# Optimization experiments

Hardware: AMD Instinct MI355X
Metric: run time of the kernel (lower is better)

## Reference

```python
import jax, jax.numpy as jnp
import numpy as np

# block index -> upsample target resolution / whether self-attention is applied
RES = [32, 64, 256, 128, 64, 32, 16, 16, 32, 64, 128, 256]
ATTN = [False, False, False, False, False, True, True, True, True, False, False, False]
EPS = 1e-5


def conv5(x, w, b):
    # valid 5x5 conv, NCHW
    y = jax.lax.conv_general_dilated(x, w, (1, 1), 'VALID',
                                     dimension_numbers=('NCHW', 'OIHW', 'NCHW'))
    return y + b[None, :, None, None]


def up_nearest(x, size):
    # torch nn.Upsample(size) nearest: src_idx = floor(dst_idx * in / out)
    H, W = x.shape[2], x.shape[3]
    ri = (jnp.arange(size) * H) // size
    ci = (jnp.arange(size) * W) // size
    return x[:, :, ri][:, :, :, ci]


def norm_hw(x):
    # InstanceNorm2d(affine=False) == LayerNorm((H,W)) with identity affine:
    # normalize over spatial dims per (N, C), biased variance.
    m = x.mean((2, 3), keepdims=True)
    v = x.var((2, 3), keepdims=True)
    return (x - m) * jax.lax.rsqrt(v + EPS)


def norm_batch(x):
    # BatchNorm2d in training mode: batch statistics over (N, H, W) per channel.
    m = x.mean((0, 2, 3), keepdims=True)
    v = x.var((0, 2, 3), keepdims=True)
    return (x - m) * jax.lax.rsqrt(v + EPS)


def attention(x, qw, qb, kw, kb, vw, vb):
    B, C, H, W = x.shape
    q = (jnp.einsum('oc,bchw->bohw', qw, x) + qb[None, :, None, None]).reshape(B, C, H * W)
    k = (jnp.einsum('oc,bchw->bohw', kw, x) + kb[None, :, None, None]).reshape(B, C, H * W)
    v = (jnp.einsum('oc,bchw->bohw', vw, x) + vb[None, :, None, None]).reshape(B, C, H * W)
    # scores[b, m, n] = sum_c k[b, c, m] * q[b, c, n]; softmax over n
    a = jax.nn.softmax(jnp.einsum('bcm,bcn->bmn', k, q), axis=-1)  # [B, HW, HW]
    out = jnp.einsum('bcm,bmn->bcn', v, a).reshape(B, C, H, W)
    return out + x


def setup_inputs() -> dict:
    key = jax.random.key(0)
    k = jax.random.split(key, 22)
    s = 0.1
    f = jnp.float32
    return {
        'x': jax.random.normal(k[0], (32, 3, 256, 256), f),
        'noise_z': jax.random.normal(k[1], (1, 512), f),
        'lin_w': jax.random.normal(k[2], (768, 512), f) * 0.02,
        'lin_b': jax.random.normal(k[3], (768,), f) * 0.02,
        'conv_w': jax.random.normal(k[4], (12, 3, 3, 5, 5), f) * s,
        'conv_b': jax.random.normal(k[5], (12, 3), f) * s,
        'conv2_w': jax.random.normal(k[6], (12, 3, 3, 5, 5), f) * s,
        'conv2_b': jax.random.normal(k[7], (12, 3), f) * s,
        'q_w': jax.random.normal(k[8], (12, 3, 3), f) * s,
        'q_b': jax.random.normal(k[9], (12, 3), f) * s,
        'k_w': jax.random.normal(k[10], (12, 3, 3), f) * s,
        'k_b': jax.random.normal(k[11], (12, 3), f) * s,
        'v_w': jax.random.normal(k[12], (12, 3, 3), f) * s,
        'v_b': jax.random.normal(k[13], (12, 3), f) * s,
        'in_p': jax.random.uniform(k[14], (12, 3), f),
        'ln_p': jax.random.uniform(k[15], (12, 3), f),
        'bn_p': jax.random.uniform(k[16], (12, 3), f),
        'bn_w': jax.random.uniform(k[17], (12, 3), f),
        'bn_b': jax.random.uniform(k[18], (12, 3), f) * 0.1,
        'p1': jax.random.uniform(k[19], (12,), f),
        'p2': jax.random.uniform(k[20], (12,), f),
    }


def reference(x, noise_z, lin_w, lin_b, conv_w, conv_b, conv2_w, conv2_b,
              q_w, q_b, k_w, k_b, v_w, v_b, in_p, ln_p, bn_p, bn_w, bn_b, p1, p2):

    def block(i, h):
        r = RES[i]
        real = h
        y = up_nearest(conv5(real, conv_w[i], conv_b[i]), r)
        # InstanceNorm / LayerNorm (no affine) coincide here; BatchNorm has affine.
        inorm = norm_hw(y)
        bnorm = norm_batch(y) * bn_w[i][None, :, None, None] + bn_b[i][None, :, None, None]
        y2 = y + (jnp.sum(in_p[i]) + jnp.sum(ln_p[i])) * inorm + jnp.sum(bn_p[i]) * bnorm
        y2 = y2 * p1[i] + p2[i] * up_nearest(conv5(real, conv2_w[i], conv2_b[i]), r)
        if ATTN[i]:
            y2 = attention(y2, q_w[i], q_b[i], k_w[i], k_b[i], v_w[i], v_b[i])
        return y2

    # noise path: Linear(512 -> 768) -> (1, 3, 16, 16) -> ReesBlock(32) -> ReesBlock(64)
    n = (noise_z @ lin_w.T + lin_b).reshape(1, 3, 16, 16)
    n = block(0, n)
    n = block(1, n)  # (1, 3, 64, 64)

    a = x
    for i in range(2, 12):
        a = block(i, a)
        if i == 4:  # encoder index 2, resolution 64 -> add noise (broadcast over batch)
            a = a + n
    return jnp.tanh(a)
```

## Files before the change

kernel.cpp:

```cpp
#include <hip/hip_runtime.h>
#include <math.h>

#define EPS 1e-5f
#define LOG2E 1.44269504088896340736f

#define AS_GLOBAL __attribute__((address_space(1)))
#define AS_LDS    __attribute__((address_space(3)))

__device__ __forceinline__ float2 ab_from(float s1, float s2, float bs, float bs2,
    float hw, float Nf, float si_, float sb, float bnw_c, float bnb_c, float p1v) {
  float inv = 1.0f / hw;
  float mi = s1 * inv, vi = s2 * inv - mi * mi;
  float ri = rsqrtf(vi + EPS);
  float invb = 1.0f / (Nf * hw);
  float mb = bs * invb, vb = bs2 * invb - mb * mb;
  float rb = rsqrtf(vb + EPS);
  float A = 1.0f + si_ * ri + sb * rb * bnw_c;
  float B = -(si_ * ri * mi + sb * rb * bnw_c * mb) + sb * bnb_c;
  return make_float2(A * p1v, B * p1v);
}

__device__ __forceinline__ void compute_AB_P(
    const float* __restrict__ P, int n, int NT, int T, float hw, float Nf,
    const float* __restrict__ inp, const float* __restrict__ lnp,
    const float* __restrict__ bnp, const float* __restrict__ bnw,
    const float* __restrict__ bnb, const float* __restrict__ p1p,
    const float* __restrict__ p2p, float* pA, float* pB, float* pP2,
    float* sred ) {
  int t = threadIdx.x;
  if (t == 0) *pP2 = p2p[0];
  if (t < 192) {
    int c2 = t >> 5, l = t & 31;
    const float* pp = P + c2 * NT;
    float aAll = 0.f, aOwn = 0.f;
    int base = n * T;
    #pragma unroll 4
    for (int i = l; i < NT; i += 32) {
      float v = pp[i];
      aAll += v;
      if ((unsigned)(i - base) < (unsigned)T) aOwn += v;
    }
    #pragma unroll
    for (int off = 16; off; off >>= 1) {
      aAll += __shfl_down(aAll, off, 32);
      aOwn += __shfl_down(aOwn, off, 32);
    }
    if (l == 0) { sred[c2] = aOwn; sred[6 + c2] = aAll; }
  }
  __syncthreads();
  if (t < 3) {
    int c = t;
    float si_ = inp[0] + inp[1] + inp[2] + lnp[0] + lnp[1] + lnp[2];
    float sb = bnp[0] + bnp[1] + bnp[2];
    float2 ab = ab_from(sred[2 * c], sred[2 * c + 1], sred[6 + 2 * c],
                        sred[6 + 2 * c + 1], hw, Nf, si_, sb, bnw[c], bnb[c],
                        p1p[0]);
    pA[c] = ab.x;
    pB[c] = ab.y;
  }
  __syncthreads();
}

#define STATS_REDUCE_STORE(scv, sqv, sumsp, bidv)                             \
  {                                                                           \
    _Pragma("unroll")                                                         \
    for (int off = 32; off; off >>= 1) {                                      \
      _Pragma("unroll")                                                       \
      for (int c = 0; c < 3; ++c) {                                           \
        scv[c] += __shfl_down(scv[c], off);                                   \
        sqv[c] += __shfl_down(sqv[c], off);                                   \
      }                                                                       \
    }                                                                         \
    __shared__ float redS[4][3], redQ[4][3];                                  \
    int wid = threadIdx.x >> 6, lane = threadIdx.x & 63;                      \
    if (lane == 0) {                                                          \
      _Pragma("unroll")                                                       \
      for (int c = 0; c < 3; ++c) { redS[wid][c] = scv[c]; redQ[wid][c] = sqv[c]; } \
    }                                                                         \
    __syncthreads();                                                          \
    if (threadIdx.x < 3) {                                                    \
      int c = threadIdx.x;                                                    \
      int NTg = (int)gridDim.x;                                               \
      sumsp[(2 * c) * NTg + (bidv)] =                                         \
          redS[0][c] + redS[1][c] + redS[2][c] + redS[3][c];                  \
      sumsp[(2 * c + 1) * NTg + (bidv)] =                                     \
          redQ[0][c] + redQ[1][c] + redQ[2][c] + redQ[3][c];                  \
    }                                                                         \
  }

__device__ __forceinline__ int xcd_swz() {
  return ((int)(blockIdx.x & 7)) * ((int)gridDim.x >> 3) + ((int)blockIdx.x >> 3);
}

template <int MODE, bool IDENT>
__device__ __forceinline__ void stage_tile(
    float* __restrict__ lin, const float* __restrict__ inb, size_t ps,
    const float2* __restrict__ pyu, size_t pbase,
    int Hin, int sy0, int sx0, int Sp, int logrp,
    const float* pA, const float* pB, float pP2v,
    const float* __restrict__ pnoise) {
  const int IW = 68, IH = 20;
  int colt = threadIdx.x & 63;
  int r4 = threadIdx.x >> 6;
  int gx = sx0 + colt; gx = gx < Hin ? gx : Hin - 1;
  int gxs = (MODE == 1) ? (IDENT ? gx : ((gx * Sp) >> logrp)) : 0;
  #pragma unroll
  for (int cc = 0; cc < 3; ++cc) {
    #pragma unroll
    for (int rb = 0; rb < 5; ++rb) {
      int rr = r4 + (rb << 2);
      int gy = sy0 + rr; gy = gy < Hin ? gy : Hin - 1;
      float val;
      if (MODE == 1) {
        int rbase = IDENT ? gy * Sp : ((gy * Sp) >> logrp) * Sp;
        float2 v = pyu[pbase + (size_t)cc * Sp * Sp + rbase + gxs];
        val = pA[cc] * v.x + pB[cc] + pP2v * v.y;
        if (pnoise) val += pnoise[((size_t)cc * Hin + gy) * Hin + gx];
      } else if (MODE == 2) {
        size_t idx = ((size_t)cc * Hin + gy) * Hin + gx;
        val = inb[idx] + inb[idx + ps] + inb[idx + 2 * ps] + inb[idx + 3 * ps];
      } else {
        val = inb[((size_t)cc * Hin + gy) * Hin + gx];
      }
      lin[(cc * IH + rr) * IW + colt] = val;
    }
  }
  if (threadIdx.x < 240) {
    int col2 = 64 + (threadIdx.x & 3);
    int rowlin = threadIdx.x >> 2;
    int cc = rowlin / 20, rr = rowlin - cc * 20;
    int gx2 = sx0 + col2; gx2 = gx2 < Hin ? gx2 : Hin - 1;
    int gy = sy0 + rr; gy = gy < Hin ? gy : Hin - 1;
    float val;
    if (MODE == 1) {
      int gxs2 = IDENT ? gx2 : ((gx2 * Sp) >> logrp);
      int rbase = IDENT ? gy * Sp : ((gy * Sp) >> logrp) * Sp;
      float2 v = pyu[pbase + (size_t)cc * Sp * Sp + rbase + gxs2];
      val = pA[cc] * v.x + pB[cc] + pP2v * v.y;
      if (pnoise) val += pnoise[((size_t)cc * Hin + gy) * Hin + gx2];
    } else if (MODE == 2) {
      size_t idx = ((size_t)cc * Hin + gy) * Hin + gx2;
      val = inb[idx] + inb[idx + ps] + inb[idx + 2 * ps] + inb[idx + 3 * ps];
    } else {
      val = inb[((size_t)cc * Hin + gy) * Hin + gx2];
    }
    lin[(cc * IH + rr) * IW + col2] = val;
  }
}

template <bool FUSED, bool SUM4>
__global__ __launch_bounds__(256) void conv_up_t(
    const float* __restrict__ in, const float2* __restrict__ pyu,
    float2* __restrict__ yu,
    const float* __restrict__ w1, const float* __restrict__ b1,
    const float* __restrict__ w2, const float* __restrict__ b2,
    float* __restrict__ sums, int Hin, int S, int r, int tilesX, int tilesY,
    const float* __restrict__ psums,
    const float* __restrict__ pinp, const float* __restrict__ plnp,
    const float* __restrict__ pbnp, const float* __restrict__ pbnw,
    const float* __restrict__ pbnb, const float* __restrict__ pp1,
    const float* __restrict__ pp2, const float* __restrict__ pnoise,
    int pN, int Sp, int logrp, int pNT, int pT) {
  const int TW = 64, TH = 16, IW = 68, IH = 20;
  __shared__ float lin[3 * IH * IW];
  __shared__ float pA[3], pB[3], pP2v, sred[12];
  int bid = xcd_swz();
  int tpi = tilesX * tilesY;
  int n = bid / tpi;
  int trem = bid - n * tpi;
  int tyB = trem / tilesX, txB = trem - tyB * tilesX;
  int px0 = txB * TW, py0 = tyB * TH;
  const float* inb = in + (size_t)n * 3 * Hin * Hin;
  if (FUSED) {
    compute_AB_P(psums, n, pNT, pT, (float)(Hin * Hin), (float)pN, pinp, plnp,
                 pbnp, pbnw, pbnb, pp1, pp2, pA, pB, &pP2v, sred);
    size_t pbase = (size_t)n * 3 * Sp * Sp;
    stage_tile<1, false>(lin, nullptr, 0, pyu, pbase, Hin, py0, px0, Sp, logrp,
                         pA, pB, pP2v, pnoise);
  } else if (SUM4) {
    size_t ps = (size_t)96 * Hin * Hin;
    stage_tile<2, false>(lin, inb, ps, nullptr, 0, Hin, py0, px0, 0, 0,
                         nullptr, nullptr, 0.f, nullptr);
  } else {
    if (px0 + IW <= Hin && py0 + IH <= Hin) {
      for (int t4 = threadIdx.x; t4 < 3 * IH * 17; t4 += 256) {
        int cc = t4 / (IH * 17);
        int rem = t4 - cc * (IH * 17);
        int rr = rem / 17, j = rem - rr * 17;
        const float* src = inb + ((size_t)cc * Hin + py0 + rr) * Hin + px0 + 4 * j;
        int base = t4 - (threadIdx.x & 63);
        __builtin_amdgcn_global_load_lds(
            (const AS_GLOBAL void*)src,
            (AS_LDS void*)(lin + 4 * base), 16, 0, 0);
      }
    } else {
      stage_tile<0, false>(lin, inb, 0, nullptr, 0, Hin, py0, px0, 0, 0,
                           nullptr, nullptr, 0.f, nullptr);
    }
  }
  __syncthreads();
  int tx = threadIdx.x & 15, ty = threadIdx.x >> 4;
  int lx0 = tx * 4;
  int px = px0 + lx0, py = py0 + ty;
  float a1[3][4], a2[3][4];
  #pragma unroll
  for (int c = 0; c < 3; ++c) {
    float bb1 = b1[c], bb2 = b2[c];
    #pragma unroll
    for (int x = 0; x < 4; ++x) { a1[c][x] = bb1; a2[c][x] = bb2; }
  }
  #pragma unroll 1
  for (int ci = 0; ci < 3; ++ci) {
    const float* lrow = lin + ci * IH * IW + ty * IW + lx0;
    float v[5][8];
    #pragma unroll
    for (int ky = 0; ky < 5; ++ky) {
      #pragma unroll
      for (int j = 0; j < 8; ++j) v[ky][j] = lrow[ky * IW + j];
    }
    const float* wp1 = w1 + ci * 25;
    const float* wp2 = w2 + ci * 25;
    #pragma unroll
    for (int ky = 0; ky < 5; ++ky) {
      #pragma unroll
      for (int c = 0; c < 3; ++c) {
        #pragma unroll
        for (int kx = 0; kx < 5; ++kx) {
          float wa = wp1[c * 75 + ky * 5 + kx];
          float wb = wp2[c * 75 + ky * 5 + kx];
          #pragma unroll
          for (int x = 0; x < 4; ++x) {
            a1[c][x] = fmaf(v[ky][kx + x], wa, a1[c][x]);
            a2[c][x] = fmaf(v[ky][kx + x], wb, a2[c][x]);
          }
        }
      }
    }
  }
  float sc[3] = {0.f, 0.f, 0.f}, sq[3] = {0.f, 0.f, 0.f};
  bool valid = (py < S) && (px < S);
  if (valid) {
    int hc = S;
    float wy = (float)(((py + 1) * r + hc - 1) / hc - (py * r + hc - 1) / hc);
    float wx[4];
    #pragma unroll
    for (int x = 0; x < 4; ++x) {
      int pxx = px + x;
      wx[x] = (float)(((pxx + 1) * r + hc - 1) / hc - (pxx * r + hc - 1) / hc);
    }
    #pragma unroll
    for (int c = 0; c < 3; ++c) {
      size_t idx = ((size_t)(n * 3 + c) * S + py) * S + px;
      float2* yp = yu + idx;
      *reinterpret_cast<float4*>(yp) =
          make_float4(a1[c][0], a2[c][0], a1[c][1], a2[c][1]);
      *reinterpret_cast<float4*>(yp + 2) =
          make_float4(a1[c][2], a2[c][2], a1[c][3], a2[c][3]);
      #pragma unroll
      for (int x = 0; x < 4; ++x) {
        float wgt = wy * wx[x];
        sc[c] += a1[c][x] * wgt;
        sq[c] += a1[c][x] * a1[c][x] * wgt;
      }
    }
  }
  STATS_REDUCE_STORE(sc, sq, sums, bid)
}

template <bool FUSED, bool IDENT, bool SUM4>
__global__ __launch_bounds__(256) void conv_dn_t(
    const float* __restrict__ in, const float2* __restrict__ pyu,
    float2* __restrict__ yu,
    const float* __restrict__ w1, const float* __restrict__ b1,
    const float* __restrict__ w2, const float* __restrict__ b2,
    float* __restrict__ sums, int Hin, int S, int hc, int logr,
    int tilesX, int tilesY,
    const float* __restrict__ psums,
    const float* __restrict__ pinp, const float* __restrict__ plnp,
    const float* __restrict__ pbnp, const float* __restrict__ pbnw,
    const float* __restrict__ pbnb, const float* __restrict__ pp1,
    const float* __restrict__ pp2, const float* __restrict__ pnoise,
    int pN, int Sp, int logrp, int pNT, int pT) {
  const int TW = 32, TH = 8, IW = 68, IH = 20;
  __shared__ float lin[3 * IH * IW];
  __shared__ float pA[3], pB[3], pP2v, sred[12];
  int bid = xcd_swz();
  int tpi = tilesX * tilesY;
  int n = bid / tpi;
  int trem = bid - n * tpi;
  int tyB = trem / tilesX, txB = trem - tyB * tilesX;
  int px0 = txB * TW, py0 = tyB * TH;
  int sy0 = (py0 * hc) >> logr, sx0 = (px0 * hc) >> logr;
  const float* inb = in + (size_t)n * 3 * Hin * Hin;
  if (FUSED) {
    compute_AB_P(psums, n, pNT, pT, (float)(Hin * Hin), (float)pN, pinp, plnp,
                 pbnp, pbnw, pbnb, pp1, pp2, pA, pB, &pP2v, sred);
    size_t pbase = (size_t)n * 3 * Sp * Sp;
    stage_tile<1, IDENT>(lin, nullptr, 0, pyu, pbase, Hin, sy0, sx0, Sp, logrp,
                         pA, pB, pP2v, pnoise);
  } else if (SUM4) {
    size_t ps = (size_t)96 * Hin * Hin;
    stage_tile<2, false>(lin, inb, ps, nullptr, 0, Hin, sy0, sx0, 0, 0,
                         nullptr, nullptr, 0.f, nullptr);
  } else {
    stage_tile<0, false>(lin, inb, 0, nullptr, 0, Hin, sy0, sx0, 0, 0,
                         nullptr, nullptr, 0.f, nullptr);
  }
  __syncthreads();
  int tx = threadIdx.x & 31, ty = threadIdx.x >> 5;
  int px = px0 + tx, py = py0 + ty;
  int sxl = ((px * hc) >> logr) - sx0;
  int syl = ((py * hc) >> logr) - sy0;
  float a1[3], a2[3];
  #pragma unroll
  for (int c = 0; c < 3; ++c) { a1[c] = b1[c]; a2[c] = b2[c]; }
  #pragma unroll
  for (int ci = 0; ci < 3; ++ci) {
    const float* lrow = lin + ci * IH * IW + syl * IW + sxl;
    const float* wp1 = w1 + ci * 25;
    const float* wp2 = w2 + ci * 25;
    #pragma unroll
    for (int ky = 0; ky < 5; ++ky) {
      float v[5];
      #pragma unroll
      for (int j = 0; j < 5; ++j) v[j] = lrow[ky * IW + j];
      #pragma unroll
      for (int c = 0; c < 3; ++c) {
        #pragma unroll
        for (int kx = 0; kx < 5; ++kx) {
          a1[c] = fmaf(v[kx], wp1[c * 75 + ky * 5 + kx], a1[c]);
          a2[c] = fmaf(v[kx], wp2[c * 75 + ky * 5 + kx], a2[c]);
        }
      }
    }
  }
  float sc[3] = {0.f, 0.f, 0.f}, sq[3] = {0.f, 0.f, 0.f};
  bool valid = (py < S) && (px < S);
  if (valid) {
    #pragma unroll
    for (int c = 0; c < 3; ++c) {
      size_t idx = ((size_t)(n * 3 + c) * S + py) * S + px;
      yu[idx] = make_float2(a1[c], a2[c]);
      sc[c] += a1[c];
      sq[c] += a1[c] * a1[c];
    }
  }
  STATS_REDUCE_STORE(sc, sq, sums, bid)
}

__global__ __launch_bounds__(256) void linear_wave(
    const float* __restrict__ z, const float* __restrict__ w,
    const float* __restrict__ b, float* __restrict__ out) {
  int row = (blockIdx.x << 2) + (threadIdx.x >> 6);
  int lane = threadIdx.x & 63;
  const float4* wr = reinterpret_cast<const float4*>(w + (size_t)row * 512);
  const float4* zz = reinterpret_cast<const float4*>(z);
  float acc = 0.f;
  #pragma unroll
  for (int i = 0; i < 2; ++i) {
    float4 wv = wr[lane + 64 * i];
    float4 zv = zz[lane + 64 * i];
    acc += wv.x * zv.x + wv.y * zv.y + wv.z * zv.z + wv.w * zv.w;
  }
  #pragma unroll
  for (int off = 32; off; off >>= 1) acc += __shfl_down(acc, off);
  if (lane == 0) out[row] = acc + b[row];
}

__global__ __launch_bounds__(256) void noise_rest(
    const float* __restrict__ L0g,
    const float* __restrict__ cw, const float* __restrict__ cb,
    const float* __restrict__ c2w, const float* __restrict__ c2b,
    const float* __restrict__ inp, const float* __restrict__ lnp,
    const float* __restrict__ bnp, const float* __restrict__ bnw,
    const float* __restrict__ bnb, const float* __restrict__ p1p,
    const float* __restrict__ p2p, float* __restrict__ nb0) {
  __shared__ float L0[768];
  __shared__ float ys0[432], u20[432];
  __shared__ float buf1[3072];
  __shared__ float ys1[2352], u21[2352];
  __shared__ float redS[4][3], redQ[4][3];
  __shared__ float AB[6];
  int tid = threadIdx.x;
  for (int t = tid; t < 768; t += 256) L0[t] = L0g[t];
  __syncthreads();
  {
    float sc[3] = {0, 0, 0}, sq[3] = {0, 0, 0};
    for (int p = tid; p < 144; p += 256) {
      int py = p / 12, px = p - py * 12;
      float a1[3], a2[3];
      #pragma unroll
      for (int c = 0; c < 3; ++c) { a1[c] = cb[c]; a2[c] = c2b[c]; }
      for (int ci = 0; ci < 3; ++ci)
        #pragma unroll
        for (int ky = 0; ky < 5; ++ky) {
          const float* row = &L0[ci * 256 + (py + ky) * 16 + px];
          #pragma unroll
          for (int c = 0; c < 3; ++c)
            #pragma unroll
            for (int kx = 0; kx < 5; ++kx) {
              a1[c] = fmaf(row[kx], cw[c * 75 + ci * 25 + ky * 5 + kx], a1[c]);
              a2[c] = fmaf(row[kx], c2w[c * 75 + ci * 25 + ky * 5 + kx], a2[c]);
            }
        }
      int wy = ((py + 1) * 32 + 11) / 12 - (py * 32 + 11) / 12;
      int wx = ((px + 1) * 32 + 11) / 12 - (px * 32 + 11) / 12;
      float wgt = (float)(wy * wx);
      #pragma unroll
      for (int c = 0; c < 3; ++c) {
        ys0[c * 144 + p] = a1[c];
        u20[c * 144 + p] = a2[c];
        sc[c] += a1[c] * wgt;
        sq[c] += a1[c] * a1[c] * wgt;
      }
    }
    #pragma unroll
    for (int off = 32; off; off >>= 1)
      #pragma unroll
      for (int c = 0; c < 3; ++c) {
        sc[c] += __shfl_down(sc[c], off);
        sq[c] += __shfl_down(sq[c], off);
      }
    int wid = tid >> 6, lane = tid & 63;
    if (lane == 0)
      #pragma unroll
      for (int c = 0; c < 3; ++c) { redS[wid][c] = sc[c]; redQ[wid][c] = sq[c]; }
    __syncthreads();
// ... 358 lines not shown
      float4 mm = mm4[j], ll = ll4[j];
      float s, w;
      s = ka.x * q0 + kbv.x * q1 + kc.x * q2;
      w = exp2f(s - mm.x) * ll.x;
      a0 = fmaf(va.x, w, a0); a1 = fmaf(vbv.x, w, a1); a2 = fmaf(vc.x, w, a2);
      s = ka.y * q0 + kbv.y * q1 + kc.y * q2;
      w = exp2f(s - mm.y) * ll.y;
      a0 = fmaf(va.y, w, a0); a1 = fmaf(vbv.y, w, a1); a2 = fmaf(vc.y, w, a2);
      s = ka.z * q0 + kbv.z * q1 + kc.z * q2;
      w = exp2f(s - mm.z) * ll.z;
      a0 = fmaf(va.z, w, a0); a1 = fmaf(vbv.z, w, a1); a2 = fmaf(vc.z, w, a2);
      s = ka.w * q0 + kbv.w * q1 + kc.w * q2;
      w = exp2f(s - mm.w) * ll.w;
      a0 = fmaf(va.w, w, a0); a1 = fmaf(vbv.w, w, a1); a2 = fmaf(vc.w, w, a2);
    }
    Oq[tid] = a0;
    Oq[1024 + tid] = a1;
    Oq[2048 + tid] = a2;
  }
  __syncthreads();
  if (tid < 768) {
    int c = tid >> 8, n = tid & 255;
    int cb_ = c << 10;
    y2s[tid] += Oq[cb_ + n] + Oq[cb_ + 256 + n] + Oq[cb_ + 512 + n] + Oq[cb_ + 768 + n];
  }
  __syncthreads();
  float sc[3] = {0.f, 0.f, 0.f}, sq[3] = {0.f, 0.f, 0.f};
  int p = tid;
  if (p < 144) {
    int py = p / 12, px = p - py * 12;
    float a1[3], a2[3];
    #pragma unroll
    for (int c = 0; c < 3; ++c) { a1[c] = cb1[c]; a2[c] = cb2[c]; }
    #pragma unroll
    for (int ci = 0; ci < 3; ++ci) {
      #pragma unroll
      for (int ky = 0; ky < 5; ++ky) {
        const float* row = &y2s[ci * 256 + (py + ky) * 16 + px];
        #pragma unroll
        for (int c = 0; c < 3; ++c) {
          #pragma unroll
          for (int kx = 0; kx < 5; ++kx) {
            a1[c] = fmaf(row[kx], cw1[c * 75 + ci * 25 + ky * 5 + kx], a1[c]);
            a2[c] = fmaf(row[kx], cw2[c * 75 + ci * 25 + ky * 5 + kx], a2[c]);
          }
        }
      }
    }
    float wy = (float)(((py + 1) * r + 11) / 12 - (py * r + 11) / 12);
    float wx = (float)(((px + 1) * r + 11) / 12 - (px * r + 11) / 12);
    float wgt = wy * wx;
    #pragma unroll
    for (int c = 0; c < 3; ++c) {
      yu_out[(size_t)(b * 3 + c) * 144 + p] = make_float2(a1[c], a2[c]);
      sc[c] += a1[c] * wgt;
      sq[c] += a1[c] * a1[c] * wgt;
    }
  }
  #pragma unroll
  for (int off = 32; off; off >>= 1) {
    #pragma unroll
    for (int c = 0; c < 3; ++c) {
      sc[c] += __shfl_down(sc[c], off);
      sq[c] += __shfl_down(sq[c], off);
    }
  }
  int wid = tid >> 6, lane = tid & 63;
  if (lane == 0) {
    #pragma unroll
    for (int c = 0; c < 3; ++c) { redS[wid][c] = sc[c]; redQ[wid][c] = sq[c]; }
  }
  __syncthreads();
  if (tid < 3) {
    int c = tid;
    float s1 = 0.f, s2 = 0.f;
    #pragma unroll
    for (int w = 0; w < 16; ++w) { s1 += redS[w][c]; s2 += redQ[w][c]; }
    int NTg = (int)gridDim.x;
    sums_out[(2 * c) * NTg + b] = s1;
    sums_out[(2 * c + 1) * NTg + b] = s2;
  }
}

__global__ __launch_bounds__(256) void elem_final(
    const float2* __restrict__ yu, const float* __restrict__ sums,
    const float* __restrict__ inp, const float* __restrict__ lnp,
    const float* __restrict__ bnp, const float* __restrict__ bnw,
    const float* __restrict__ bnb, const float* __restrict__ p1p,
    const float* __restrict__ p2p, float* __restrict__ out, int S,
    int pNT, int pT) {
  __shared__ float pA[3], pB[3], pP2v, sred[12];
  int bid = xcd_swz();
  int n = bid >> 8;
  int p = ((bid & 255) << 8) + threadIdx.x;
  compute_AB_P(sums, n, pNT, pT, 65536.f, 32.f, inp, lnp, bnp, bnw, bnb, p1p,
               p2p, pA, pB, &pP2v, sred);
  int oy = p >> 8, ox = p & 255;
  int si = ((oy * S) >> 8) * S + ((ox * S) >> 8);
  size_t ybase = (size_t)n * 3 * S * S;
  #pragma unroll
  for (int c = 0; c < 3; ++c) {
    float2 v = yu[ybase + c * S * S + si];
    out[((size_t)(n * 3 + c) << 16) + p] = tanhf(pA[c] * v.x + pB[c] + pP2v * v.y);
  }
}

#define NPX nullptr, nullptr, nullptr, nullptr, nullptr, nullptr, nullptr, \
            nullptr, nullptr, 0, 0, 0, 0, 0

extern "C" void kernel_launch(void* const* d_in, const int* in_sizes, int n_in,
                              void* d_out, int out_size, void* d_ws, size_t ws_size,
                              hipStream_t stream) {
  const float* x       = (const float*)d_in[0];
  const float* noise_z = (const float*)d_in[1];
  const float* lin_w   = (const float*)d_in[2];
  const float* lin_b   = (const float*)d_in[3];
  const float* conv_w  = (const float*)d_in[4];
  const float* conv_b  = (const float*)d_in[5];
  const float* conv2_w = (const float*)d_in[6];
  const float* conv2_b = (const float*)d_in[7];
  const float* q_w     = (const float*)d_in[8];
  const float* q_b     = (const float*)d_in[9];
  const float* k_w     = (const float*)d_in[10];
  const float* k_b     = (const float*)d_in[11];
  const float* v_w     = (const float*)d_in[12];
  const float* v_b     = (const float*)d_in[13];
  const float* in_p    = (const float*)d_in[14];
  const float* ln_p    = (const float*)d_in[15];
  const float* bn_p    = (const float*)d_in[16];
  const float* bn_w    = (const float*)d_in[17];
  const float* bn_b    = (const float*)d_in[18];
  const float* p1      = (const float*)d_in[19];
  const float* p2      = (const float*)d_in[20];
  float* out = (float*)d_out;

  float* ws = (float*)d_ws;
  size_t off = 0;
  auto alloc = [&](size_t nf) { float* p = ws + off; off += nf; return p; };
  float* PS   = alloc(33408);
  float* PS2  = PS;
  float* PS3  = PS + 12288;
  float* PS4  = PS + 24576;
  float* PS5  = PS + 27648;
  float* PS6  = PS + 28416;
  float* PS6a = PS + 28800;
  float* PS7a = PS + 28992;
  float* PS9  = PS + 29184;
  float* PS10 = PS + 29568;
  float* PS11 = PS + 30336;
  float* P45  = alloc(393216);
  float* P48  = alloc(393216);
  float2* YU2 = (float2*)alloc(12192768);
  float2* PA  = (float2*)alloc(3145728);
  float2* PB  = (float2*)alloc(3145728);
  float* Mp   = alloc(131072);
  float* Lp   = alloc(131072);
  float* NB0  = alloc(12288);
  float* LIN  = alloc(768);

  const float* nul = nullptr;
  const float2* nul2 = nullptr;

  linear_wave<<<192, 256, 0, stream>>>(noise_z, lin_w, lin_b, LIN);
  noise_rest<<<1, 256, 0, stream>>>(LIN, conv_w, conv_b, conv2_w, conv2_b,
      in_p, ln_p, bn_p, bn_w, bn_b, p1, p2, NB0);

  conv_up_t<false, false><<<2048, 256, 0, stream>>>(x, nul2, YU2, conv_w + 450,
      conv_b + 6, conv2_w + 450, conv2_b + 6, PS2, 256, 252, 256, 4, 16,
      NPX);
  conv_dn_t<true, false, false><<<2048, 256, 0, stream>>>(nul, YU2, PA,
      conv_w + 675, conv_b + 9, conv2_w + 675, conv2_b + 9, PS3,
      256, 128, 252, 7, 4, 16,
      PS2, in_p + 6, ln_p + 6, bn_p + 6, bn_w + 6, bn_b + 6, p1 + 2,
      p2 + 2, nul, 32, 252, 8, 2048, 64);
  conv_dn_t<true, true, false><<<512, 256, 0, stream>>>(nul, PA, PB,
      conv_w + 900, conv_b + 12, conv2_w + 900, conv2_b + 12, PS4,
      128, 64, 124, 6, 2, 8,
      PS3, in_p + 9, ln_p + 9, bn_p + 9, bn_w + 9, bn_b + 9, p1 + 3,
      p2 + 3, nul, 32, 128, 7, 2048, 64);
  conv_dn_t<true, true, false><<<128, 256, 0, stream>>>(nul, PB, PA,
      conv_w + 1125, conv_b + 15, conv2_w + 1125, conv2_b + 15, PS5,
      64, 32, 60, 5, 1, 4,
      PS4, in_p + 12, ln_p + 12, bn_p + 12, bn_w + 12, bn_b + 12, p1 + 4,
      p2 + 4, NB0, 32, 64, 6, 512, 16);
  attn_rows_f<<<512, 256, 0, stream>>>(PA, PS5, in_p + 15, ln_p + 15,
      bn_p + 15, bn_w + 15, bn_b + 15, p1 + 5, p2 + 5,
      q_w + 45, q_b + 15, k_w + 45, k_b + 15, Mp, Lp, 32, 128, 4);
  attn_out_f<<<512, 256, 0, stream>>>(PA, PS5, in_p + 15, ln_p + 15,
      bn_p + 15, bn_w + 15, bn_b + 15, p1 + 5, p2 + 5,
      q_w + 45, q_b + 15, k_w + 45, k_b + 15, v_w + 45, v_b + 15, Mp, Lp, P45,
      32, 128, 4);
  conv_dn_t<false, false, true><<<64, 256, 0, stream>>>(P45, nul2, PB,
      conv_w + 1350, conv_b + 18, conv2_w + 1350, conv2_b + 18, PS6,
      32, 16, 28, 4, 1, 2, NPX);
  attn256_conv<<<32, 1024, 0, stream>>>(PB, PS6, in_p + 18, ln_p + 18,
      bn_p + 18, bn_w + 18, bn_b + 18, p1 + 6, p2 + 6,
      q_w + 54, q_b + 18, k_w + 54, k_b + 18, v_w + 54, v_b + 18,
      conv_w + 1575, conv_b + 21, conv2_w + 1575, conv2_b + 21,
      PA, PS6a, 16, 16, 64, 2);
  attn256_conv<<<32, 1024, 0, stream>>>(PA, PS6a, in_p + 21, ln_p + 21,
      bn_p + 21, bn_w + 21, bn_b + 21, p1 + 7, p2 + 7,
      q_w + 63, q_b + 21, k_w + 63, k_b + 21, v_w + 63, v_b + 21,
      conv_w + 1800, conv_b + 24, conv2_w + 1800, conv2_b + 24,
      PB, PS7a, 12, 32, 32, 1);
  attn_rows_f<<<512, 256, 0, stream>>>(PB, PS7a, in_p + 24, ln_p + 24,
      bn_p + 24, bn_w + 24, bn_b + 24, p1 + 8, p2 + 8,
      q_w + 72, q_b + 24, k_w + 72, k_b + 24, Mp, Lp, 12, 32, 1);
  attn_out_f<<<512, 256, 0, stream>>>(PB, PS7a, in_p + 24, ln_p + 24,
      bn_p + 24, bn_w + 24, bn_b + 24, p1 + 8, p2 + 8,
      q_w + 72, q_b + 24, k_w + 72, k_b + 24, v_w + 72, v_b + 24, Mp, Lp, P48,
      12, 32, 1);
  conv_up_t<false, true><<<64, 256, 0, stream>>>(P48, nul2, PA, conv_w + 2025,
      conv_b + 27, conv2_w + 2025, conv2_b + 27, PS9, 32, 28, 64, 1, 2,
      NPX);
  conv_up_t<true, false><<<128, 256, 0, stream>>>(nul, PA, PB, conv_w + 2250,
      conv_b + 30, conv2_w + 2250, conv2_b + 30, PS10, 64, 60, 128, 1, 4,
      PS9, in_p + 27, ln_p + 27, bn_p + 27, bn_w + 27, bn_b + 27,
      p1 + 9, p2 + 9, nul, 32, 28, 6, 64, 2);
  conv_up_t<true, false><<<512, 256, 0, stream>>>(nul, PB, YU2, conv_w + 2475,
      conv_b + 33, conv2_w + 2475, conv2_b + 33, PS11, 128, 124, 256, 2, 8,
      PS10, in_p + 30, ln_p + 30, bn_p + 30, bn_w + 30, bn_b + 30,
      p1 + 10, p2 + 10, nul, 32, 60, 7, 128, 4);
  elem_final<<<8192, 256, 0, stream>>>(YU2, PS11, in_p + 33, ln_p + 33,
      bn_p + 33, bn_w + 33, bn_b + 33, p1 + 11, p2 + 11, out, 124, 512, 16);
}
```

Before: 442.1 us.

## Attend at 12x12 source resolution with multiplicity weights and enlarge conv tiles

Block 8's attention runs on the 32x32 nearest-upsampled map, whose values come from a 12x12 source. A new single-block-per-batch attn144 kernel computes attention on the 144 unique positions, weighting each key by its replication count, and writes a 12x12 output. The following upsample conv stage (new stage mode 3) reads that small map through the nearest index mapping, replacing the two 1024-wide attention kernels and the large intermediate buffer. Separately, the first two full-resolution conv kernels now compute 32 or 16 output rows per block (multiple rows per thread), halving the grid and the number of partial-stat slots, in exchange for more registers per thread.

```diff
diff --git a/kernel.cpp b/kernel.cpp
--- a/kernel.cpp
+++ b/kernel.cpp
@@ -93,62 +93,65 @@
 }
 
 template <int MODE, bool IDENT>
+__device__ __forceinline__ float stage_val(
+    const float* __restrict__ inb, size_t ps,
+    const float2* __restrict__ pyu, size_t pbase,
+    int Hin, int gy, int gx, int Sp, int logrp,
+    const float* pA, const float* pB, float pP2v,
+    const float* __restrict__ pnoise, int cc) {
+  if (MODE == 1) {
+    int gxs = IDENT ? gx : ((gx * Sp) >> logrp);
+    int rbase = IDENT ? gy * Sp : ((gy * Sp) >> logrp) * Sp;
+    float2 v = pyu[pbase + (size_t)cc * Sp * Sp + rbase + gxs];
+    float val = pA[cc] * v.x + pB[cc] + pP2v * v.y;
+    if (pnoise) val += pnoise[((size_t)cc * Hin + gy) * Hin + gx];
+    return val;
+  } else if (MODE == 2) {
+    size_t idx = ((size_t)cc * Hin + gy) * Hin + gx;
+    return inb[idx] + inb[idx + ps] + inb[idx + 2 * ps] + inb[idx + 3 * ps];
+  } else if (MODE == 3) {
+    int gys = (gy * Sp) >> logrp, gxs = (gx * Sp) >> logrp;
+    return inb[(cc * Sp + gys) * Sp + gxs];
+  } else {
+    return inb[((size_t)cc * Hin + gy) * Hin + gx];
+  }
+}
+
+template <int MODE, bool IDENT, int IHv>
 __device__ __forceinline__ void stage_tile(
     float* __restrict__ lin, const float* __restrict__ inb, size_t ps,
     const float2* __restrict__ pyu, size_t pbase,
     int Hin, int sy0, int sx0, int Sp, int logrp,
     const float* pA, const float* pB, float pP2v,
     const float* __restrict__ pnoise) {
-  const int IW = 68, IH = 20;
+  const int IW = 68;
   int colt = threadIdx.x & 63;
   int r4 = threadIdx.x >> 6;
   int gx = sx0 + colt; gx = gx < Hin ? gx : Hin - 1;
-  int gxs = (MODE == 1) ? (IDENT ? gx : ((gx * Sp) >> logrp)) : 0;
   #pragma unroll
   for (int cc = 0; cc < 3; ++cc) {
     #pragma unroll
-    for (int rb = 0; rb < 5; ++rb) {
+    for (int rb = 0; rb < IHv / 4; ++rb) {
       int rr = r4 + (rb << 2);
       int gy = sy0 + rr; gy = gy < Hin ? gy : Hin - 1;
-      float val;
-      if (MODE == 1) {
-        int rbase = IDENT ? gy * Sp : ((gy * Sp) >> logrp) * Sp;
-        float2 v = pyu[pbase + (size_t)cc * Sp * Sp + rbase + gxs];
-        val = pA[cc] * v.x + pB[cc] + pP2v * v.y;
-        if (pnoise) val += pnoise[((size_t)cc * Hin + gy) * Hin + gx];
-      } else if (MODE == 2) {
-        size_t idx = ((size_t)cc * Hin + gy) * Hin + gx;
-        val = inb[idx] + inb[idx + ps] + inb[idx + 2 * ps] + inb[idx + 3 * ps];
-      } else {
-        val = inb[((size_t)cc * Hin + gy) * Hin + gx];
-      }
-      lin[(cc * IH + rr) * IW + colt] = val;
-    }
-  }
-  if (threadIdx.x < 240) {
-    int col2 = 64 + (threadIdx.x & 3);
-    int rowlin = threadIdx.x >> 2;
-    int cc = rowlin / 20, rr = rowlin - cc * 20;
+      lin[(cc * IHv + rr) * IW + colt] =
+          stage_val<MODE, IDENT>(inb, ps, pyu, pbase, Hin, gy, gx, Sp, logrp,
+                                 pA, pB, pP2v, pnoise, cc);
+    }
+  }
+  for (int t = threadIdx.x; t < 3 * IHv * 4; t += 256) {
+    int col2 = 64 + (t & 3);
+    int rowlin = t >> 2;
+    int cc = rowlin / IHv, rr = rowlin - cc * IHv;
     int gx2 = sx0 + col2; gx2 = gx2 < Hin ? gx2 : Hin - 1;
     int gy = sy0 + rr; gy = gy < Hin ? gy : Hin - 1;
-    float val;
-    if (MODE == 1) {
-      int gxs2 = IDENT ? gx2 : ((gx2 * Sp) >> logrp);
-      int rbase = IDENT ? gy * Sp : ((gy * Sp) >> logrp) * Sp;
-      float2 v = pyu[pbase + (size_t)cc * Sp * Sp + rbase + gxs2];
-      val = pA[cc] * v.x + pB[cc] + pP2v * v.y;
-      if (pnoise) val += pnoise[((size_t)cc * Hin + gy) * Hin + gx2];
-    } else if (MODE == 2) {
-      size_t idx = ((size_t)cc * Hin + gy) * Hin + gx2;
-      val = inb[idx] + inb[idx + ps] + inb[idx + 2 * ps] + inb[idx + 3 * ps];
-    } else {
-      val = inb[((size_t)cc * Hin + gy) * Hin + gx2];
-    }
-    lin[(cc * IH + rr) * IW + col2] = val;
-  }
-}
-
-template <bool FUSED, bool SUM4>
+    lin[(cc * IHv + rr) * IW + col2] =
+        stage_val<MODE, IDENT>(inb, ps, pyu, pbase, Hin, gy, gx2, Sp, logrp,
+                               pA, pB, pP2v, pnoise, cc);
+  }
+}
+
+template <int SMODE, int THv>
 __global__ __launch_bounds__(256) void conv_up_t(
     const float* __restrict__ in, const float2* __restrict__ pyu,
     float2* __restrict__ yu,
@@ -161,7 +164,7 @@
     const float* __restrict__ pbnb, const float* __restrict__ pp1,
     const float* __restrict__ pp2, const float* __restrict__ pnoise,
     int pN, int Sp, int logrp, int pNT, int pT) {
-  const int TW = 64, TH = 16, IW = 68, IH = 20;
+  const int TW = 64, IW = 68, IH = THv + 4, NH = THv / 16;
   __shared__ float lin[3 * IH * IW];
   __shared__ float pA[3], pB[3], pP2v, sred[12];
   int bid = xcd_swz();
@@ -169,18 +172,18 @@
   int n = bid / tpi;
   int trem = bid - n * tpi;
   int tyB = trem / tilesX, txB = trem - tyB * tilesX;
-  int px0 = txB * TW, py0 = tyB * TH;
+  int px0 = txB * TW, py0 = tyB * THv;
   const float* inb = in + (size_t)n * 3 * Hin * Hin;
-  if (FUSED) {
+  if (SMODE == 1) {
     compute_AB_P(psums, n, pNT, pT, (float)(Hin * Hin), (float)pN, pinp, plnp,
                  pbnp, pbnw, pbnb, pp1, pp2, pA, pB, &pP2v, sred);
     size_t pbase = (size_t)n * 3 * Sp * Sp;
-    stage_tile<1, false>(lin, nullptr, 0, pyu, pbase, Hin, py0, px0, Sp, logrp,
-                         pA, pB, pP2v, pnoise);
-  } else if (SUM4) {
-    size_t ps = (size_t)96 * Hin * Hin;
-    stage_tile<2, false>(lin, inb, ps, nullptr, 0, Hin, py0, px0, 0, 0,
-                         nullptr, nullptr, 0.f, nullptr);
+    stage_tile<1, false, IH>(lin, nullptr, 0, pyu, pbase, Hin, py0, px0, Sp,
+                             logrp, pA, pB, pP2v, pnoise);
+  } else if (SMODE == 3) {
+    const float* smallb = in + (size_t)n * 3 * Sp * Sp;
+    stage_tile<3, false, IH>(lin, smallb, 0, nullptr, 0, Hin, py0, px0, Sp,
+                             logrp, nullptr, nullptr, 0.f, nullptr);
   } else {
     if (px0 + IW <= Hin && py0 + IH <= Hin) {
       for (int t4 = threadIdx.x; t4 < 3 * IH * 17; t4 += 256) {
@@ -194,80 +197,90 @@
             (AS_LDS void*)(lin + 4 * base), 16, 0, 0);
       }
     } else {
-      stage_tile<0, false>(lin, inb, 0, nullptr, 0, Hin, py0, px0, 0, 0,
-                           nullptr, nullptr, 0.f, nullptr);
+      stage_tile<0, false, IH>(lin, inb, 0, nullptr, 0, Hin, py0, px0, 0, 0,
+                               nullptr, nullptr, 0.f, nullptr);
     }
   }
   __syncthreads();
   int tx = threadIdx.x & 15, ty = threadIdx.x >> 4;
   int lx0 = tx * 4;
-  int px = px0 + lx0, py = py0 + ty;
-  float a1[3][4], a2[3][4];
-  #pragma unroll
-  for (int c = 0; c < 3; ++c) {
-    float bb1 = b1[c], bb2 = b2[c];
-    #pragma unroll
-    for (int x = 0; x < 4; ++x) { a1[c][x] = bb1; a2[c][x] = bb2; }
+  float a1[NH][3][4], a2[NH][3][4];
+  #pragma unroll
+  for (int h = 0; h < NH; ++h) {
+    #pragma unroll
+    for (int c = 0; c < 3; ++c) {
+      float bb1 = b1[c], bb2 = b2[c];
+      #pragma unroll
+      for (int x = 0; x < 4; ++x) { a1[h][c][x] = bb1; a2[h][c][x] = bb2; }
+    }
   }
   #pragma unroll 1
   for (int ci = 0; ci < 3; ++ci) {
-    const float* lrow = lin + ci * IH * IW + ty * IW + lx0;
-    float v[5][8];
-    #pragma unroll
-    for (int ky = 0; ky < 5; ++ky) {
-      #pragma unroll
-      for (int j = 0; j < 8; ++j) v[ky][j] = lrow[ky * IW + j];
-    }
     const float* wp1 = w1 + ci * 25;
     const float* wp2 = w2 + ci * 25;
     #pragma unroll
-    for (int ky = 0; ky < 5; ++ky) {
-      #pragma unroll
-      for (int c = 0; c < 3; ++c) {
+    for (int h = 0; h < NH; ++h) {
+      const float* lrow = lin + (ci * IH + ty + 16 * h) * IW + lx0;
+      float v[5][8];
+      #pragma unroll
+      for (int ky = 0; ky < 5; ++ky) {
         #pragma unroll
-        for (int kx = 0; kx < 5; ++kx) {
-          float wa = wp1[c * 75 + ky * 5 + kx];
-          float wb = wp2[c * 75 + ky * 5 + kx];
+        for (int j = 0; j < 8; ++j) v[ky][j] = lrow[ky * IW + j];
+      }
+      #pragma unroll
+      for (int ky = 0; ky < 5; ++ky) {
+        #pragma unroll
+        for (int c = 0; c < 3; ++c) {
           #pragma unroll
-          for (int x = 0; x < 4; ++x) {
-            a1[c][x] = fmaf(v[ky][kx + x], wa, a1[c][x]);
-            a2[c][x] = fmaf(v[ky][kx + x], wb, a2[c][x]);
+          for (int kx = 0; kx < 5; ++kx) {
+            float wa = wp1[c * 75 + ky * 5 + kx];
+            float wb = wp2[c * 75 + ky * 5 + kx];
+            #pragma unroll
+            for (int x = 0; x < 4; ++x) {
+              a1[h][c][x] = fmaf(v[ky][kx + x], wa, a1[h][c][x]);
+              a2[h][c][x] = fmaf(v[ky][kx + x], wb, a2[h][c][x]);
+            }
           }
         }
       }
     }
   }
   float sc[3] = {0.f, 0.f, 0.f}, sq[3] = {0.f, 0.f, 0.f};
-  bool valid = (py < S) && (px < S);
-  if (valid) {
-    int hc = S;
-    float wy = (float)(((py + 1) * r + hc - 1) / hc - (py * r + hc - 1) / hc);
-    float wx[4];
-    #pragma unroll
-    for (int x = 0; x < 4; ++x) {
-      int pxx = px + x;
-      wx[x] = (float)(((pxx + 1) * r + hc - 1) / hc - (pxx * r + hc - 1) / hc);
-    }
-    #pragma unroll
-    for (int c = 0; c < 3; ++c) {
-      size_t idx = ((size_t)(n * 3 + c) * S + py) * S + px;
-      float2* yp = yu + idx;
-      *reinterpret_cast<float4*>(yp) =
-          make_float4(a1[c][0], a2[c][0], a1[c][1], a2[c][1]);
-      *reinterpret_cast<float4*>(yp + 2) =
-          make_float4(a1[c][2], a2[c][2], a1[c][3], a2[c][3]);
+  int hc = S;
+  int px = px0 + lx0;
+  #pragma unroll
+  for (int h = 0; h < NH; ++h) {
+    int py = py0 + ty + 16 * h;
+    bool valid = (py < S) && (px < S);
+    if (valid) {
+      float wy = (float)(((py + 1) * r + hc - 1) / hc - (py * r + hc - 1) / hc);
+      float wx[4];
       #pragma unroll
       for (int x = 0; x < 4; ++x) {
-        float wgt = wy * wx[x];
-        sc[c] += a1[c][x] * wgt;
-        sq[c] += a1[c][x] * a1[c][x] * wgt;
+        int pxx = px + x;
+        wx[x] = (float)(((pxx + 1) * r + hc - 1) / hc - (pxx * r + hc - 1) / hc);
       }
+      #pragma unroll
+      for (int c = 0; c < 3; ++c) {
+        size_t idx = ((size_t)(n * 3 + c) * S + py) * S + px;
+        float2* yp = yu + idx;
+        *reinterpret_cast<float4*>(yp) =
+            make_float4(a1[h][c][0], a2[h][c][0], a1[h][c][1], a2[h][c][1]);
+        *reinterpret_cast<float4*>(yp + 2) =
+            make_float4(a1[h][c][2], a2[h][c][2], a1[h][c][3], a2[h][c][3]);
+        #pragma unroll
+        for (int x = 0; x < 4; ++x) {
+          float wgt = wy * wx[x];
+          sc[c] += a1[h][c][x] * wgt;
+          sq[c] += a1[h][c][x] * a1[h][c][x] * wgt;
+        }
+      }
     }
   }
   STATS_REDUCE_STORE(sc, sq, sums, bid)
 }
 
-template <bool FUSED, bool IDENT, bool SUM4>
+template <int SMODE, bool IDENT, int THv>
 __global__ __launch_bounds__(256) void conv_dn_t(
     const float* __restrict__ in, const float2* __restrict__ pyu,
     float2* __restrict__ yu,
@@ -281,7 +294,7 @@
     const float* __restrict__ pbnb, const float* __restrict__ pp1,
     const float* __restrict__ pp2, const float* __restrict__ pnoise,
     int pN, int Sp, int logrp, int pNT, int pT) {
-  const int TW = 32, TH = 8, IW = 68, IH = 20;
+  const int TW = 32, IW = 68, IH = (THv == 16) ? 36 : 20, NH = THv / 8;
   __shared__ float lin[3 * IH * IW];
   __shared__ float pA[3], pB[3], pP2v, sred[12];
   int bid = xcd_swz();
@@ -289,60 +302,73 @@
   int n = bid / tpi;
   int trem = bid - n * tpi;
   int tyB = trem / tilesX, txB = trem - tyB * tilesX;
-  int px0 = txB * TW, py0 = tyB * TH;
+  int px0 = txB * TW, py0 = tyB * THv;
   int sy0 = (py0 * hc) >> logr, sx0 = (px0 * hc) >> logr;
   const float* inb = in + (size_t)n * 3 * Hin * Hin;
-  if (FUSED) {
+  if (SMODE == 1) {
     compute_AB_P(psums, n, pNT, pT, (float)(Hin * Hin), (float)pN, pinp, plnp,
                  pbnp, pbnw, pbnb, pp1, pp2, pA, pB, &pP2v, sred);
     size_t pbase = (size_t)n * 3 * Sp * Sp;
-    stage_tile<1, IDENT>(lin, nullptr, 0, pyu, pbase, Hin, sy0, sx0, Sp, logrp,
-                         pA, pB, pP2v, pnoise);
-  } else if (SUM4) {
+    stage_tile<1, IDENT, IH>(lin, nullptr, 0, pyu, pbase, Hin, sy0, sx0, Sp,
+                             logrp, pA, pB, pP2v, pnoise);
+  } else if (SMODE == 2) {
     size_t ps = (size_t)96 * Hin * Hin;
-    stage_tile<2, false>(lin, inb, ps, nullptr, 0, Hin, sy0, sx0, 0, 0,
-                         nullptr, nullptr, 0.f, nullptr);
+    stage_tile<2, false, IH>(lin, inb, ps, nullptr, 0, Hin, sy0, sx0, 0, 0,
+                             nullptr, nullptr, 0.f, nullptr);
   } else {
-    stage_tile<0, false>(lin, inb, 0, nullptr, 0, Hin, sy0, sx0, 0, 0,
-                         nullptr, nullptr, 0.f, nullptr);
+    stage_tile<0, false, IH>(lin, inb, 0, nullptr, 0, Hin, sy0, sx0, 0, 0,
+                             nullptr, nullptr, 0.f, nullptr);
   }
   __syncthreads();
   int tx = threadIdx.x & 31, ty = threadIdx.x >> 5;
-  int px = px0 + tx, py = py0 + ty;
+  int px = px0 + tx;
   int sxl = ((px * hc) >> logr) - sx0;
-  int syl = ((py * hc) >> logr) - sy0;
-  float a1[3], a2[3];
-  #pragma unroll
-  for (int c = 0; c < 3; ++c) { a1[c] = b1[c]; a2[c] = b2[c]; }
+  int pys[NH], syl[NH];
+  #pragma unroll
+  for (int h = 0; h < NH; ++h) {
+    pys[h] = py0 + ty + 8 * h;
+    syl[h] = ((pys[h] * hc) >> logr) - sy0;
+  }
+  float a1[NH][3], a2[NH][3];
+  #pragma unroll
+  for (int h = 0; h < NH; ++h)
+    #pragma unroll
+    for (int c = 0; c < 3; ++c) { a1[h][c] = b1[c]; a2[h][c] = b2[c]; }
   #pragma unroll
   for (int ci = 0; ci < 3; ++ci) {
-    const float* lrow = lin + ci * IH * IW + syl * IW + sxl;
     const float* wp1 = w1 + ci * 25;
     const float* wp2 = w2 + ci * 25;
     #pragma unroll
-    for (int ky = 0; ky < 5; ++ky) {
-      float v[5];
-      #pragma unroll
-      for (int j = 0; j < 5; ++j) v[j] = lrow[ky * IW + j];
-      #pragma unroll
-      for (int c = 0; c < 3; ++c) {
+    for (int h = 0; h < NH; ++h) {
+      const float* lrow = lin + (ci * IH + syl[h]) * IW + sxl;
+      #pragma unroll
+      for (int ky = 0; ky < 5; ++ky) {
+        float v[5];
         #pragma unroll
-        for (int kx = 0; kx < 5; ++kx) {
-          a1[c] = fmaf(v[kx], wp1[c * 75 + ky * 5 + kx], a1[c]);
-          a2[c] = fmaf(v[kx], wp2[c * 75 + ky * 5 + kx], a2[c]);
+        for (int j = 0; j < 5; ++j) v[j] = lrow[ky * IW + j];
+        #pragma unroll
+        for (int c = 0; c < 3; ++c) {
+          #pragma unroll
+          for (int kx = 0; kx < 5; ++kx) {
+            a1[h][c] = fmaf(v[kx], wp1[c * 75 + ky * 5 + kx], a1[h][c]);
+            a2[h][c] = fmaf(v[kx], wp2[c * 75 + ky * 5 + kx], a2[h][c]);
+          }
         }
       }
     }
   }
   float sc[3] = {0.f, 0.f, 0.f}, sq[3] = {0.f, 0.f, 0.f};
-  bool valid = (py < S) && (px < S);
-  if (valid) {
-    #pragma unroll
-    for (int c = 0; c < 3; ++c) {
-      size_t idx = ((size_t)(n * 3 + c) * S + py) * S + px;
-      yu[idx] = make_float2(a1[c], a2[c]);
-      sc[c] += a1[c];
-      sq[c] += a1[c] * a1[c];
+  #pragma unroll
+  for (int h = 0; h < NH; ++h) {
+    bool valid = (pys[h] < S) && (px < S);
+    if (valid) {
+      #pragma unroll
+      for (int c = 0; c < 3; ++c) {
+        size_t idx = ((size_t)(n * 3 + c) * S + pys[h]) * S + px;
+        yu[idx] = make_float2(a1[h][c], a2[h][c]);
+        sc[c] += a1[h][c];
+        sq[c] += a1[h][c] * a1[h][c];
+      }
     }
   }
   STATS_REDUCE_STORE(sc, sq, sums, bid)
@@ -867,6 +893,79 @@
   }
 }
 
+__global__ __launch_bounds__(256) void attn144(
+    const float2* __restrict__ yu, const float* __restrict__ sums,
+    const float* __restrict__ inp, const float* __restrict__ lnp,
+    const float* __restrict__ bnp, const float* __restrict__ bnw,
+    const float* __restrict__ bnb, const float* __restrict__ p1p,
+    const float* __restrict__ p2p,
+    const float* __restrict__ qw, const float* __restrict__ qb,
+    const float* __restrict__ kw, const float* __restrict__ kb,
+    const float* __restrict__ vw, const float* __restrict__ vb,
+    float* __restrict__ O) {
+  __shared__ float pA[3], pB[3], pP2v, sred[12];
+  __shared__ float y2[432], qs[432], ks[432], vs[432];
+  __shared__ float Ms[144], Ls[144], wn[144];
+  int b = blockIdx.x;
+  int tid = threadIdx.x;
+  compute_AB_P(sums, b, 32, 1, 1024.f, 32.f, inp, lnp, bnp, bnw, bnb, p1p,
+               p2p, pA, pB, &pP2v, sred);
+  for (int t = tid; t < 432; t += 256) {
+    int c = t / 144, j = t - c * 144;
+    float2 v = yu[((size_t)b * 3 + c) * 144 + j];
+    y2[t] = pA[c] * v.x + pB[c] + pP2v * v.y;
+  }
+  __syncthreads();
+  if (tid < 144) {
+    int j = tid;
+    float y0 = y2[j], y1 = y2[144 + j], y2v = y2[288 + j];
+    #pragma unroll
+    for (int o = 0; o < 3; ++o) {
+      qs[o * 144 + j] = qb[o] + qw[o * 3] * y0 + qw[o * 3 + 1] * y1 + qw[o * 3 + 2] * y2v;
+      ks[o * 144 + j] = (kb[o] + kw[o * 3] * y0 + kw[o * 3 + 1] * y1 + kw[o * 3 + 2] * y2v) * LOG2E;
+      vs[o * 144 + j] = vb[o] + vw[o * 3] * y0 + vw[o * 3 + 1] * y1 + vw[o * 3 + 2] * y2v;
+    }
+    int jy = j / 12, jx = j - jy * 12;
+    int cy = (8 * (jy + 1) + 2) / 3 - (8 * jy + 2) / 3;
+    int cx = (8 * (jx + 1) + 2) / 3 - (8 * jx + 2) / 3;
+    wn[j] = (float)(cy * cx);
+  }
+  __syncthreads();
+  if (tid < 144) {
+    int m = tid;
+    float kx = ks[m], ky = ks[144 + m], kz = ks[288 + m];
+    float mr = -1e30f;
+    for (int nn = 0; nn < 144; ++nn) {
+      float s = kx * qs[nn] + ky * qs[144 + nn] + kz * qs[288 + nn];
+      mr = fmaxf(mr, s);
+    }
+    float l = 0.f;
+    for (int nn = 0; nn < 144; ++nn) {
+      float s = kx * qs[nn] + ky * qs[144 + nn] + kz * qs[288 + nn];
+      l += wn[nn] * exp2f(s - mr);
+    }
+    Ms[m] = mr;
+    Ls[m] = 1.0f / l;
+  }
+  __syncthreads();
+  if (tid < 144) {
+    int nq = tid;
+    float q0 = qs[nq], q1 = qs[144 + nq], q2 = qs[288 + nq];
+    float a0 = 0.f, a1 = 0.f, a2 = 0.f;
+    for (int m = 0; m < 144; ++m) {
+      float s = ks[m] * q0 + ks[144 + m] * q1 + ks[288 + m] * q2;
+      float w = wn[m] * exp2f(s - Ms[m]) * Ls[m];
+      a0 = fmaf(vs[m], w, a0);
+      a1 = fmaf(vs[144 + m], w, a1);
+      a2 = fmaf(vs[288 + m], w, a2);
+    }
+    size_t ob = (size_t)b * 432;
+    O[ob + nq] = a0 + y2[nq];
+    O[ob + 144 + nq] = a1 + y2[144 + nq];
+    O[ob + 288 + nq] = a2 + y2[288 + nq];
+  }
+}
+
 __global__ __launch_bounds__(256) void elem_final(
     const float2* __restrict__ yu, const float* __restrict__ sums,
     const float* __restrict__ inp, const float* __restrict__ lnp,
@@ -922,19 +1021,19 @@
   float* ws = (float*)d_ws;
   size_t off = 0;
   auto alloc = [&](size_t nf) { float* p = ws + off; off += nf; return p; };
-  float* PS   = alloc(33408);
+  float* PS   = alloc(21120);
   float* PS2  = PS;
-  float* PS3  = PS + 12288;
-  float* PS4  = PS + 24576;
-  float* PS5  = PS + 27648;
-  float* PS6  = PS + 28416;
-  float* PS6a = PS + 28800;
-  float* PS7a = PS + 28992;
-  float* PS9  = PS + 29184;
-  float* PS10 = PS + 29568;
-  float* PS11 = PS + 30336;
+  float* PS3  = PS + 6144;
+  float* PS4  = PS + 12288;
+  float* PS5  = PS + 15360;
+  float* PS6  = PS + 16128;
+  float* PS6a = PS + 16512;
+  float* PS7a = PS + 16704;
+  float* PS9  = PS + 16896;
+  float* PS10 = PS + 17280;
+  float* PS11 = PS + 18048;
   float* P45  = alloc(393216);
-  float* P48  = alloc(393216);
+  float* O144 = alloc(13824);
   float2* YU2 = (float2*)alloc(12192768);
   float2* PA  = (float2*)alloc(3145728);
   float2* PB  = (float2*)alloc(3145728);
@@ -950,20 +1049,20 @@
   noise_rest<<<1, 256, 0, stream>>>(LIN, conv_w, conv_b, conv2_w, conv2_b,
       in_p, ln_p, bn_p, bn_w, bn_b, p1, p2, NB0);
 
-  conv_up_t<false, false><<<2048, 256, 0, stream>>>(x, nul2, YU2, conv_w + 450,
-      conv_b + 6, conv2_w + 450, conv2_b + 6, PS2, 256, 252, 256, 4, 16,
+  conv_up_t<0, 32><<<1024, 256, 0, stream>>>(x, nul2, YU2, conv_w + 450,
+      conv_b + 6, conv2_w + 450, conv2_b + 6, PS2, 256, 252, 256, 4, 8,
       NPX);
-  conv_dn_t<true, false, false><<<2048, 256, 0, stream>>>(nul, YU2, PA,
+  conv_dn_t<1, false, 16><<<1024, 256, 0, stream>>>(nul, YU2, PA,
       conv_w + 675, conv_b + 9, conv2_w + 675, conv2_b + 9, PS3,
-      256, 128, 252, 7, 4, 16,
+      256, 128, 252, 7, 4, 8,
       PS2, in_p + 6, ln_p + 6, bn_p + 6, bn_w + 6, bn_b + 6, p1 + 2,
-      p2 + 2, nul, 32, 252, 8, 2048, 64);
-  conv_dn_t<true, true, false><<<512, 256, 0, stream>>>(nul, PA, PB,
+      p2 + 2, nul, 32, 252, 8, 1024, 32);
+  conv_dn_t<1, true, 8><<<512, 256, 0, stream>>>(nul, PA, PB,
       conv_w + 900, conv_b + 12, conv2_w + 900, conv2_b + 12, PS4,
       128, 64, 124, 6, 2, 8,
       PS3, in_p + 9, ln_p + 9, bn_p + 9, bn_w + 9, bn_b + 9, p1 + 3,
-      p2 + 3, nul, 32, 128, 7, 2048, 64);
-  conv_dn_t<true, true, false><<<128, 256, 0, stream>>>(nul, PB, PA,
+      p2 + 3, nul, 32, 128, 7, 1024, 32);
+  conv_dn_t<1, true, 8><<<128, 256, 0, stream>>>(nul, PB, PA,
       conv_w + 1125, conv_b + 15, conv2_w + 1125, conv2_b + 15, PS5,
       64, 32, 60, 5, 1, 4,
       PS4, in_p + 12, ln_p + 12, bn_p + 12, bn_w + 12, bn_b + 12, p1 + 4,
@@ -975,7 +1074,7 @@
       bn_p + 15, bn_w + 15, bn_b + 15, p1 + 5, p2 + 5,
       q_w + 45, q_b + 15, k_w + 45, k_b + 15, v_w + 45, v_b + 15, Mp, Lp, P45,
       32, 128, 4);
-  conv_dn_t<false, false, true><<<64, 256, 0, stream>>>(P45, nul2, PB,
+  conv_dn_t<2, false, 8><<<64, 256, 0, stream>>>(P45, nul2, PB,
       conv_w + 1350, conv_b + 18, conv2_w + 1350, conv2_b + 18, PS6,
       32, 16, 28, 4, 1, 2, NPX);
   attn256_conv<<<32, 1024, 0, stream>>>(PB, PS6, in_p + 18, ln_p + 18,
@@ -988,21 +1087,18 @@
       q_w + 63, q_b + 21, k_w + 63, k_b + 21, v_w + 63, v_b + 21,
       conv_w + 1800, conv_b + 24, conv2_w + 1800, conv2_b + 24,
       PB, PS7a, 12, 32, 32, 1);
-  attn_rows_f<<<512, 256, 0, stream>>>(PB, PS7a, in_p + 24, ln_p + 24,
+  attn144<<<32, 256, 0, stream>>>(PB, PS7a, in_p + 24, ln_p + 24,
       bn_p + 24, bn_w + 24, bn_b + 24, p1 + 8, p2 + 8,
-      q_w + 72, q_b + 24, k_w + 72, k_b + 24, Mp, Lp, 12, 32, 1);
-  attn_out_f<<<512, 256, 0, stream>>>(PB, PS7a, in_p + 24, ln_p + 24,
-      bn_p + 24, bn_w + 24, bn_b + 24, p1 + 8, p2 + 8,
-      q_w + 72, q_b + 24, k_w + 72, k_b + 24, v_w + 72, v_b + 24, Mp, Lp, P48,
-      12, 32, 1);
-  conv_up_t<false, true><<<64, 256, 0, stream>>>(P48, nul2, PA, conv_w + 2025,
+      q_w + 72, q_b + 24, k_w + 72, k_b + 24, v_w + 72, v_b + 24, O144);
+  conv_up_t<3, 16><<<64, 256, 0, stream>>>(O144, nul2, PA, conv_w + 2025,
       conv_b + 27, conv2_w + 2025, conv2_b + 27, PS9, 32, 28, 64, 1, 2,
-      NPX);
-  conv_up_t<true, false><<<128, 256, 0, stream>>>(nul, PA, PB, conv_w + 2250,
+      nullptr, nullptr, nullptr, nullptr, nullptr, nullptr, nullptr,
+      nullptr, nullptr, 0, 12, 5, 0, 0);
+  conv_up_t<1, 16><<<128, 256, 0, stream>>>(nul, PA, PB, conv_w + 2250,
       conv_b + 30, conv2_w + 2250, conv2_b + 30, PS10, 64, 60, 128, 1, 4,
       PS9, in_p + 27, ln_p + 27, bn_p + 27, bn_w + 27, bn_b + 27,
       p1 + 9, p2 + 9, nul, 32, 28, 6, 64, 2);
-  conv_up_t<true, false><<<512, 256, 0, stream>>>(nul, PB, YU2, conv_w + 2475,
+  conv_up_t<1, 16><<<512, 256, 0, stream>>>(nul, PB, YU2, conv_w + 2475,
       conv_b + 33, conv2_w + 2475, conv2_b + 33, PS11, 128, 124, 256, 2, 8,
       PS10, in_p + 30, ln_p + 30, bn_p + 30, bn_w + 30, bn_b + 30,
       p1 + 10, p2 + 10, nul, 32, 60, 7, 128, 4);
```

Result: no change. 434.1 us (-1.8%).
